# Optimization experiments

Measured on AMD Instinct MI355X. Metric: run time of the kernel, lower is better.

The kernel has to match this reference:

```python
import jax, jax.numpy as jnp
import numpy as np

B, S, V, E, H, T = 256, 160, 50000, 300, 256, 200

def setup_inputs() -> dict:
    key = jax.random.key(0)
    ks = jax.random.split(key, 12)
    return {
        'x1': jax.random.randint(ks[0], (B, S), 0, V),
        'x2': jax.random.randint(ks[1], (B, S), 0, V),
        'x1mask': jnp.ones((B, S), jnp.float32),
        'key_c': jax.random.normal(ks[2], (B, S, T), jnp.float32) * 0.1,
        'key_r': jax.random.normal(ks[3], (B, S, T), jnp.float32) * 0.1,
        'emb_table': jax.random.normal(ks[4], (V, E), jnp.float32) * 0.1,
        'W_ih': jax.random.normal(ks[5], (4 * H, E), jnp.float32) * 0.05,
        'W_hh': jax.random.normal(ks[6], (4 * H, H), jnp.float32) * 0.05,
        'W_kh': jax.random.normal(ks[7], (4 * H, T), jnp.float32) * 0.05,
        'b_g': jnp.zeros((4 * H,), jnp.float32),
        'W_attn': jax.random.normal(ks[8], (H, H), jnp.float32) * 0.05,
        'b_attn': jnp.zeros((H,), jnp.float32),
        'M': jax.random.normal(ks[9], (H, H), jnp.float32) * 0.05,
        'b': jnp.zeros((1,), jnp.float32),
    }

def _run_rnn(x_emb, k_emb, W_ih, W_hh, W_kh, b_g):
    # x_emb: [B,S,E], k_emb: [B,S,T] -> hidden states [B,S,H]
    Bn = x_emb.shape[0]
    h0 = jnp.zeros((Bn, H), x_emb.dtype)
    c0 = jnp.zeros((Bn, H), x_emb.dtype)
    def cell(carry, inp):
        h, c = carry
        x_t, k_t = inp
        g = x_t @ W_ih.T + h @ W_hh.T + k_t @ W_kh.T + b_g  # [B,4H]
        i, f, gg, o = jnp.split(g, 4, axis=-1)
        c = jax.nn.sigmoid(f) * c + jax.nn.sigmoid(i) * jnp.tanh(gg)
        h = jax.nn.sigmoid(o) * jnp.tanh(c)
        return (h, c), h
    xs = (jnp.swapaxes(x_emb, 0, 1), jnp.swapaxes(k_emb, 0, 1))  # time-major
    (_, _), hs = jax.lax.scan(cell, (h0, c0), xs)
    return jnp.swapaxes(hs, 0, 1)  # [B,S,H]

def reference(x1, x2, x1mask, key_c, key_r, emb_table, W_ih, W_hh, W_kh, b_g,
              W_attn, b_attn, M, b):
    x1_emb = emb_table[x1]  # [B,S,E] (dropout = identity at eval)
    x2_emb = emb_table[x2]
    sc = _run_rnn(x1_emb, key_c, W_ih, W_hh, W_kh, b_g)  # context states [B,S,H]
    rs = _run_rnn(x2_emb, key_r, W_ih, W_hh, W_kh, b_g)
    r = rs[:, -1]  # last response hidden [B,H]
    # masked dot-product attention over context states keyed by r
    attn = sc @ W_attn.T + b_attn  # [B,S,H]
    energies = jnp.einsum('bsh,bh->bs', attn, r) * x1mask
    alpha = jax.nn.softmax(energies, axis=-1)
    c_attn = jnp.einsum('bs,bsh->bh', alpha, sc)
    # bilinear score
    o = jnp.einsum('bh,hk,bk->b', c_attn, M, r) + b[0]
    return o
```

## Files before the change

kernel.cpp:

```cpp
#include <hip/hip_runtime.h>
#include <math.h>

#define B_   256
#define S_   160
#define E_   300
#define H_   256
#define T_   200
#define G4H  1024
#define CH   16
#define NCH  10

typedef float  f32x4  __attribute__((ext_vector_type(4)));
typedef __bf16 bf16x4 __attribute__((ext_vector_type(4)));
typedef __bf16 bf16x8 __attribute__((ext_vector_type(8)));

__device__ __forceinline__ float sigf(float x) {
    float e = expf(-fabsf(x));
    float p = 1.0f / (1.0f + e);
    return x >= 0.0f ? p : e * p;
}

__device__ __forceinline__ int norig(int np) {
    return ((np >> 4) & 3) * 256 + ((np >> 6) << 4) + (np & 15);
}

__device__ __forceinline__ float4 pick4(const float* __restrict__ e,
                                        const float* __restrict__ k, int kg) {
    if (kg < E_)      return *(const float4*)(e + kg);
    if (kg < E_ + T_) return *(const float4*)(k + (kg - E_));
    return make_float4(0.f, 0.f, 0.f, 0.f);
}

__device__ __forceinline__ void split4(float4 v, bf16x4& h, bf16x4& l) {
    h[0] = (__bf16)v.x; l[0] = (__bf16)(v.x - (float)h[0]);
    h[1] = (__bf16)v.y; l[1] = (__bf16)(v.y - (float)h[1]);
    h[2] = (__bf16)v.z; l[2] = (__bf16)(v.z - (float)h[2]);
    h[3] = (__bf16)v.w; l[3] = (__bf16)(v.w - (float)h[3]);
}

__global__ __launch_bounds__(128) void prep_split(
    const float* __restrict__ Whh, const float* __restrict__ Wih,
    const float* __restrict__ Wkh,
    __bf16* __restrict__ whh_hi, __bf16* __restrict__ whh_lo,
    __bf16* __restrict__ wik_hi, __bf16* __restrict__ wik_lo)
{
    const int n  = blockIdx.x;
    const int np = ((n & 255) >> 4) * 64 + (n >> 8) * 16 + (n & 15);
    const int t  = threadIdx.x;
    {
        const int k4 = t * 4;
        float4 v;
        if (k4 < E_)            v = *(const float4*)(Wih + (size_t)n * E_ + k4);
        else if (k4 < E_ + T_)  v = *(const float4*)(Wkh + (size_t)n * T_ + (k4 - E_));
        else                    v = make_float4(0.f, 0.f, 0.f, 0.f);
        bf16x4 h, l;
        split4(v, h, l);
        *(bf16x4*)(wik_hi + (size_t)np * 512 + k4) = h;
        *(bf16x4*)(wik_lo + (size_t)np * 512 + k4) = l;
    }
    if (t < 64) {
        const int k4 = t * 4;
        const float4 v = *(const float4*)(Whh + (size_t)n * 256 + k4);
        bf16x4 h, l;
        split4(v, h, l);
        *(bf16x4*)(whh_hi + (size_t)np * 256 + k4) = h;
        *(bf16x4*)(whh_lo + (size_t)np * 256 + k4) = l;
    }
}

__global__ __launch_bounds__(512, 2) void gemm_g2(
    const int* __restrict__ x1, const int* __restrict__ x2,
    const float* __restrict__ key_c, const float* __restrict__ key_r,
    const float* __restrict__ emb,
    const __bf16* __restrict__ wik_hi, const __bf16* __restrict__ wik_lo,
    const float* __restrict__ bg,
    float* __restrict__ G, int s0)
{
    __shared__ __align__(16) __bf16 Ah[128 * 32];
    __shared__ __align__(16) __bf16 Al[128 * 32];
    __shared__ __align__(16) __bf16 Bh[128 * 32];
    __shared__ __align__(16) __bf16 Bl[128 * 32];

    const int t   = threadIdx.x;
    const int rnn = blockIdx.z;
    const int m0  = blockIdx.x * 128;
    const int n0  = blockIdx.y * 128;
    const int* xx = rnn ? x2 : x1;
    const float* key = rnn ? key_r : key_c;

    const int r0 = t >> 2;
    const int cq = t & 3;
    const int csw = ((cq ^ ((r0 >> 1) & 3)) * 16);

    const float* aeb; const float* akb;
    const __bf16* wph; const __bf16* wpl;
    {
        const int am = m0 + r0;
        const int bs = (am >> 4) * S_ + s0 + (am & 15);
        aeb = emb + (size_t)xx[bs] * E_;
        akb = key + (size_t)bs * T_;
        wph = wik_hi + (size_t)(n0 + r0) * 512;
        wpl = wik_lo + (size_t)(n0 + r0) * 512;
    }

    const int w  = t >> 6;
    const int wm = w >> 2;
    const int wn = w & 3;
    const int l  = t & 63;
    const int cl = l & 15;
    const int ch = l >> 4;
    const int chs = ((ch ^ ((cl >> 1) & 3)) * 16);

    f32x4 acc[4][2];
    #pragma unroll
    for (int fm = 0; fm < 4; ++fm)
        #pragma unroll
        for (int fn = 0; fn < 2; ++fn) acc[fm][fn] = (f32x4){0.f, 0.f, 0.f, 0.f};

    for (int kt = 0; kt < 16; ++kt) {
        const int kg = kt * 32 + cq * 8;
        const float4 va0 = pick4(aeb, akb, kg);
        const float4 va1 = pick4(aeb, akb, kg + 4);
        const bf16x8 vbh = *(const bf16x8*)(wph + kg);
        const bf16x8 vbl = *(const bf16x8*)(wpl + kg);
        bf16x4 h0, l0, h1, l1;
        split4(va0, h0, l0);
        split4(va1, h1, l1);
        const bf16x8 sah = __builtin_shufflevector(h0, h1, 0, 1, 2, 3, 4, 5, 6, 7);
        const bf16x8 sal = __builtin_shufflevector(l0, l1, 0, 1, 2, 3, 4, 5, 6, 7);
        __syncthreads();
        {
            const int off = r0 * 64 + csw;
            *(bf16x8*)((char*)Ah + off) = sah;
            *(bf16x8*)((char*)Al + off) = sal;
            *(bf16x8*)((char*)Bh + off) = vbh;
            *(bf16x8*)((char*)Bl + off) = vbl;
        }
        __syncthreads();

        bf16x8 fBh[2], fBl[2];
        #pragma unroll
        for (int fn = 0; fn < 2; ++fn) {
            const int off = (wn * 32 + fn * 16 + cl) * 64 + chs;
            fBh[fn] = *(const bf16x8*)((const char*)Bh + off);
            fBl[fn] = *(const bf16x8*)((const char*)Bl + off);
        }
        #pragma unroll
        for (int fm = 0; fm < 4; ++fm) {
            const int off = (wm * 64 + fm * 16 + cl) * 64 + chs;
            const bf16x8 fAh = *(const bf16x8*)((const char*)Ah + off);
            const bf16x8 fAl = *(const bf16x8*)((const char*)Al + off);
            #pragma unroll
            for (int fn = 0; fn < 2; ++fn) {
                acc[fm][fn] = __builtin_amdgcn_mfma_f32_16x16x32_bf16(fAh, fBh[fn], acc[fm][fn], 0, 0, 0);
                acc[fm][fn] = __builtin_amdgcn_mfma_f32_16x16x32_bf16(fAh, fBl[fn], acc[fm][fn], 0, 0, 0);
                acc[fm][fn] = __builtin_amdgcn_mfma_f32_16x16x32_bf16(fAl, fBh[fn], acc[fm][fn], 0, 0, 0);
            }
        }
    }

    float bgl[2];
    #pragma unroll
    for (int fn = 0; fn < 2; ++fn)
        bgl[fn] = bg[norig(n0 + wn * 32 + fn * 16 + cl)];

    #pragma unroll
    for (int fm = 0; fm < 4; ++fm) {
        #pragma unroll
        for (int r = 0; r < 4; ++r) {
            const int m  = m0 + wm * 64 + fm * 16 + ch * 4 + r;
            const int b  = m >> 4;
            const int sl = m & 15;
            float* rowp = G + ((size_t)(rnn * CH + sl) * B_ + b) * G4H;
            #pragma unroll
            for (int fn = 0; fn < 2; ++fn)
                rowp[n0 + wn * 32 + fn * 16 + cl] = acc[fm][fn][r] + bgl[fn];
        }
    }
}

__global__ __launch_bounds__(256, 2) void lstm_ks(
    const float* __restrict__ G,
    const __bf16* __restrict__ Whi, const __bf16* __restrict__ Wlo,
    const __bf16* __restrict__ hhi_in, const __bf16* __restrict__ hlo_in,
    __bf16* __restrict__ hhi_out, __bf16* __restrict__ hlo_out,
    float* __restrict__ cst, float* __restrict__ sc,
    int sl, int s_glob, int first)
{
    __shared__ float ps[64 * 66];

    const int t  = threadIdx.x;
    const int w  = t >> 6;
    const int l  = t & 63;
    const int cl = l & 15;
    const int ch = l >> 4;
    const int mt = blockIdx.x;
    const int jt = blockIdx.y;
    const int rnn = mt >> 4;
    const int b0  = (mt & 15) * 16;
    const int m0  = mt * 16;

    const int me = t >> 4;
    const int jl = t & 15;
    const int j  = jt * 16 + jl;
    float Ge[4];
    const float* Gb = G + ((size_t)(rnn * CH + sl) * B_ + b0 + me) * G4H + jt * 64;
    #pragma unroll
    for (int g = 0; g < 4; ++g) Ge[g] = Gb[g * 16 + jl];
    const float c_in = first ? 0.f : cst[(size_t)(m0 + me) * 256 + j];

    const size_t ab = (size_t)(m0 + cl) * 256 + w * 64 + ch * 8;
    const bf16x8 fAh0 = *(const bf16x8*)(hhi_in + ab);
    const bf16x8 fAh1 = *(const bf16x8*)(hhi_in + ab + 32);
    const bf16x8 fAl0 = *(const bf16x8*)(hlo_in + ab);
    const bf16x8 fAl1 = *(const bf16x8*)(hlo_in + ab + 32);

    bf16x8 fBh[4][2], fBl[4][2];
    #pragma unroll
    for (int g = 0; g < 4; ++g) {
        const size_t bb = (size_t)(jt * 64 + g * 16 + cl) * 256 + w * 64 + ch * 8;
        fBh[g][0] = *(const bf16x8*)(Whi + bb);
        fBh[g][1] = *(const bf16x8*)(Whi + bb + 32);
        fBl[g][0] = *(const bf16x8*)(Wlo + bb);
        fBl[g][1] = *(const bf16x8*)(Wlo + bb + 32);
    }

    f32x4 acc[4];
    #pragma unroll
    for (int g = 0; g < 4; ++g) acc[g] = (f32x4){0.f, 0.f, 0.f, 0.f};
    #pragma unroll
    for (int g = 0; g < 4; ++g) {
        acc[g] = __builtin_amdgcn_mfma_f32_16x16x32_bf16(fAh0, fBh[g][0], acc[g], 0, 0, 0);
        acc[g] = __builtin_amdgcn_mfma_f32_16x16x32_bf16(fAh1, fBh[g][1], acc[g], 0, 0, 0);
        acc[g] = __builtin_amdgcn_mfma_f32_16x16x32_bf16(fAh0, fBl[g][0], acc[g], 0, 0, 0);
        acc[g] = __builtin_amdgcn_mfma_f32_16x16x32_bf16(fAh1, fBl[g][1], acc[g], 0, 0, 0);
        acc[g] = __builtin_amdgcn_mfma_f32_16x16x32_bf16(fAl0, fBh[g][0], acc[g], 0, 0, 0);
        acc[g] = __builtin_amdgcn_mfma_f32_16x16x32_bf16(fAl1, fBh[g][1], acc[g], 0, 0, 0);
    }

    #pragma unroll
    for (int g = 0; g < 4; ++g)
        #pragma unroll
        for (int r = 0; r < 4; ++r)
            ps[(w * 16 + ch * 4 + r) * 66 + g * 16 + cl] = acc[g][r];
    __syncthreads();

    float g4[4];
    #pragma unroll
    for (int g = 0; g < 4; ++g) {
        float s = Ge[g];
        #pragma unroll
        for (int w2 = 0; w2 < 4; ++w2)
            s += ps[(w2 * 16 + me) * 66 + g * 16 + jl];
        g4[g] = s;
    }
    const float c = sigf(g4[1]) * c_in + sigf(g4[0]) * tanhf(g4[2]);
    const float h = sigf(g4[3]) * tanhf(c);
    cst[(size_t)(m0 + me) * 256 + j] = c;
    const __bf16 hh = (__bf16)h;
    const size_t ho = (size_t)(m0 + me) * 256 + j;
    hhi_out[ho] = hh;
    hlo_out[ho] = (__bf16)(h - (float)hh);
    if (rnn == 0)
        sc[((size_t)(b0 + me) * S_ + s_glob) * H_ + j] = h;
}

__global__ __launch_bounds__(256) void final_kernel(
    const float* __restrict__ sc,
    const __bf16* __restrict__ rhi, const __bf16* __restrict__ rlo,
    const float* __restrict__ Wattn, const float* __restrict__ battn,
    const float* __restrict__ M, const float* __restrict__ bscal,
    const float* __restrict__ mask, float* __restrict__ out)
{
    __shared__ float rs[256], us[256], red[256], as_[256];
    const int b = blockIdx.x;
    const int t = threadIdx.x;

    const size_t ri = (size_t)(256 + b) * 256 + t;
    rs[t] = (float)rhi[ri] + (float)rlo[ri];
    __syncthreads();

    float acc = 0.0f;
    for (int h = 0; h < 256; ++h) acc += rs[h] * Wattn[h * 256 + t];
    us[t] = acc;

    red[t] = battn[t] * rs[t];
    __syncthreads();
    for (int off = 128; off; off >>= 1) {
        if (t < off) red[t] += red[t + off];
        __syncthreads();
    }
    float beta = red[0];
    __syncthreads();

    float vh = 0.0f;
    {
        const float* Mrow = M + t * 256;
        for (int k = 0; k < 256; ++k) vh += Mrow[k] * rs[k];
    }

    float e = -INFINITY;
    if (t < S_) {
        float d = 0.0f;
        const float* scrow = sc + ((size_t)b * S_ + t) * H_;
        for (int h = 0; h < 256; ++h) d += scrow[h] * us[h];
        e = (d + beta) * mask[b * S_ + t];
    }
    red[t] = e;
    __syncthreads();
    for (int off = 128; off; off >>= 1) {
        if (t < off) red[t] = fmaxf(red[t], red[t + off]);
        __syncthreads();
    }
    float mx = red[0];
    __syncthreads();

    float p = (t < S_) ? expf(e - mx) : 0.0f;
    as_[t] = p;
    red[t] = p;
    __syncthreads();
    for (int off = 128; off; off >>= 1) {
        if (t < off) red[t] += red[t + off];
        __syncthreads();
    }
    float inv = 1.0f / red[0];
    __syncthreads();

    float ca = 0.0f;
    for (int s = 0; s < S_; ++s) ca += as_[s] * sc[((size_t)b * S_ + s) * H_ + t];
    ca *= inv;

    red[t] = ca * vh;
    __syncthreads();
    for (int off = 128; off; off >>= 1) {
        if (t < off) red[t] += red[t + off];
        __syncthreads();
    }
    if (t == 0) out[b] = red[0] + bscal[0];
}

extern "C" void kernel_launch(void* const* d_in, const int* in_sizes, int n_in,
                              void* d_out, int out_size, void* d_ws, size_t ws_size,
                              hipStream_t stream)
{
    const int*   x1    = (const int*)d_in[0];
    const int*   x2    = (const int*)d_in[1];
    const float* mask  = (const float*)d_in[2];
    const float* key_c = (const float*)d_in[3];
    const float* key_r = (const float*)d_in[4];
    const float* emb   = (const float*)d_in[5];
    const float* Wih   = (const float*)d_in[6];
    const float* Whh   = (const float*)d_in[7];
    const float* Wkh   = (const float*)d_in[8];
    const float* bg    = (const float*)d_in[9];
    const float* Wattn = (const float*)d_in[10];
    const float* battn = (const float*)d_in[11];
    const float* M     = (const float*)d_in[12];
    const float* bb    = (const float*)d_in[13];
    float* out = (float*)d_out;
    char*  wsb = (char*)d_ws;

    float*  G     = (float*)(wsb + 0);
    float*  sc    = (float*)(wsb + 33554432);
    __bf16* hhi0  = (__bf16*)(wsb + 75497472);
    __bf16* hlo0  = (__bf16*)(wsb + 75759616);
    __bf16* hhi1  = (__bf16*)(wsb + 76021760);
    __bf16* hlo1  = (__bf16*)(wsb + 76283904);
    float*  cst   = (float*)(wsb + 76546048);
    __bf16* WhhHi = (__bf16*)(wsb + 77070336);
    __bf16* WhhLo = (__bf16*)(wsb + 77594624);
    __bf16* WikHi = (__bf16*)(wsb + 78118912);
    __bf16* WikLo = (__bf16*)(wsb + 79167488);
    if (ws_size < 80216064) return;

    hipMemsetAsync(hhi0, 0, 524288, stream);
    prep_split<<<dim3(1024), 128, 0, stream>>>(Whh, Wih, Wkh,
                                               WhhHi, WhhLo, WikHi, WikLo);

    for (int ci = 0; ci < NCH; ++ci) {
        gemm_g2<<<dim3(32, 8, 2), 512, 0, stream>>>(x1, x2, key_c, key_r, emb,
                                                    WikHi, WikLo, bg, G, ci * CH);
        for (int slq = 0; slq < CH; ++slq) {
            const int s   = ci * CH + slq;
            const int par = s & 1;
            lstm_ks<<<dim3(32, 16), 256, 0, stream>>>(G, WhhHi, WhhLo,
                                                      par ? hhi1 : hhi0,
                                                      par ? hlo1 : hlo0,
                                                      par ? hhi0 : hhi1,
                                                      par ? hlo0 : hlo1,
                                                      cst, sc, slq, s, s == 0);
        }
    }

    final_kernel<<<dim3(256), 256, 0, stream>>>(sc, hhi0, hlo0, Wattn, battn,
                                                M, bb, mask, out);
}
```

Baseline: 1.473 ms.

## Fuse input-projection GEMM slices into recurrent step kernels via ring buffer

Replaces the chunked schedule, which ran one big input-projection GEMM per 16 steps followed by 16 recurrent-step launches, with a boot GEMM for the first 16 timesteps. After that, each step launch also computes the input projection for timestep t+16 in extra blocks, writing into a 17-slot ring buffer. The goal is to hide the GEMM work inside the latency-bound recurrent steps, which use only 512 blocks, and to remove the separate GEMM launches. The GEMM tile shrinks to 64x64 with 256 threads. The risk is that the extra GEMM blocks compete with the critical-path LSTM blocks for compute units and slow each step.

```diff
diff --git a/kernel.cpp b/kernel.cpp
--- a/kernel.cpp
+++ b/kernel.cpp
@@ -9,6 +9,9 @@
 #define G4H  1024
 #define CH   16
 #define NCH  10
+#define NSTEP 160
+#define NSLOT 17
+#define SLICE_F 524288
 
 typedef float  f32x4  __attribute__((ext_vector_type(4)));
 typedef __bf16 bf16x4 __attribute__((ext_vector_type(4)));
@@ -68,52 +71,46 @@
     }
 }
 
-__global__ __launch_bounds__(512, 2) void gemm_g2(
+__device__ __forceinline__ void dev_gemm_slice(
+    char* smem, int mx, int ny, int rnn, int s_tgt,
     const int* __restrict__ x1, const int* __restrict__ x2,
     const float* __restrict__ key_c, const float* __restrict__ key_r,
     const float* __restrict__ emb,
     const __bf16* __restrict__ wik_hi, const __bf16* __restrict__ wik_lo,
-    const float* __restrict__ bg,
-    float* __restrict__ G, int s0)
-{
-    __shared__ __align__(16) __bf16 Ah[128 * 32];
-    __shared__ __align__(16) __bf16 Al[128 * 32];
-    __shared__ __align__(16) __bf16 Bh[128 * 32];
-    __shared__ __align__(16) __bf16 Bl[128 * 32];
-
-    const int t   = threadIdx.x;
-    const int rnn = blockIdx.z;
-    const int m0  = blockIdx.x * 128;
-    const int n0  = blockIdx.y * 128;
+    const float* __restrict__ bg, float* __restrict__ Gw)
+{
+    __bf16* Ah = (__bf16*)smem;
+    __bf16* Al = Ah + 64 * 32;
+    __bf16* Bh = Al + 64 * 32;
+    __bf16* Bl = Bh + 64 * 32;
+
+    const int t  = threadIdx.x;
+    const int m0 = mx * 64;
+    const int n0 = ny * 64;
     const int* xx = rnn ? x2 : x1;
     const float* key = rnn ? key_r : key_c;
 
-    const int r0 = t >> 2;
-    const int cq = t & 3;
+    const int r0  = t >> 2;
+    const int cq  = t & 3;
     const int csw = ((cq ^ ((r0 >> 1) & 3)) * 16);
 
-    const float* aeb; const float* akb;
-    const __bf16* wph; const __bf16* wpl;
-    {
-        const int am = m0 + r0;
-        const int bs = (am >> 4) * S_ + s0 + (am & 15);
-        aeb = emb + (size_t)xx[bs] * E_;
-        akb = key + (size_t)bs * T_;
-        wph = wik_hi + (size_t)(n0 + r0) * 512;
-        wpl = wik_lo + (size_t)(n0 + r0) * 512;
-    }
+    const int bs = (m0 + r0) * S_ + s_tgt;
+    const float* aeb = emb + (size_t)xx[bs] * E_;
+    const float* akb = key + (size_t)bs * T_;
+    const __bf16* wph = wik_hi + (size_t)(n0 + r0) * 512;
+    const __bf16* wpl = wik_lo + (size_t)(n0 + r0) * 512;
 
     const int w  = t >> 6;
-    const int wm = w >> 2;
-    const int wn = w & 3;
+    const int wm = w >> 1;
+    const int wn = w & 1;
     const int l  = t & 63;
     const int cl = l & 15;
     const int ch = l >> 4;
     const int chs = ((ch ^ ((cl >> 1) & 3)) * 16);
 
-    f32x4 acc[4][2];
-    #pragma unroll
-    for (int fm = 0; fm < 4; ++fm)
+    f32x4 acc[2][2];
+    #pragma unroll
+    for (int fm = 0; fm < 2; ++fm)
         #pragma unroll
         for (int fn = 0; fn < 2; ++fn) acc[fm][fn] = (f32x4){0.f, 0.f, 0.f, 0.f};
 
@@ -146,8 +143,8 @@
             fBl[fn] = *(const bf16x8*)((const char*)Bl + off);
         }
         #pragma unroll
-        for (int fm = 0; fm < 4; ++fm) {
-            const int off = (wm * 64 + fm * 16 + cl) * 64 + chs;
+        for (int fm = 0; fm < 2; ++fm) {
+            const int off = (wm * 32 + fm * 16 + cl) * 64 + chs;
             const bf16x8 fAh = *(const bf16x8*)((const char*)Ah + off);
             const bf16x8 fAl = *(const bf16x8*)((const char*)Al + off);
             #pragma unroll
@@ -165,13 +162,11 @@
         bgl[fn] = bg[norig(n0 + wn * 32 + fn * 16 + cl)];
 
     #pragma unroll
-    for (int fm = 0; fm < 4; ++fm) {
+    for (int fm = 0; fm < 2; ++fm) {
         #pragma unroll
         for (int r = 0; r < 4; ++r) {
-            const int m  = m0 + wm * 64 + fm * 16 + ch * 4 + r;
-            const int b  = m >> 4;
-            const int sl = m & 15;
-            float* rowp = G + ((size_t)(rnn * CH + sl) * B_ + b) * G4H;
+            const int b = m0 + wm * 32 + fm * 16 + ch * 4 + r;
+            float* rowp = Gw + ((size_t)rnn * 256 + b) * G4H;
             #pragma unroll
             for (int fn = 0; fn < 2; ++fn)
                 rowp[n0 + wn * 32 + fn * 16 + cl] = acc[fm][fn][r] + bgl[fn];
@@ -179,23 +174,22 @@
     }
 }
 
-__global__ __launch_bounds__(256, 2) void lstm_ks(
-    const float* __restrict__ G,
+__device__ __forceinline__ void dev_lstm_step(
+    char* smem, int mt, int jt,
+    const float* __restrict__ Gread,
     const __bf16* __restrict__ Whi, const __bf16* __restrict__ Wlo,
     const __bf16* __restrict__ hhi_in, const __bf16* __restrict__ hlo_in,
     __bf16* __restrict__ hhi_out, __bf16* __restrict__ hlo_out,
     float* __restrict__ cst, float* __restrict__ sc,
-    int sl, int s_glob, int first)
-{
-    __shared__ float ps[64 * 66];
+    int s_glob, int first)
+{
+    float* ps = (float*)smem;
 
     const int t  = threadIdx.x;
     const int w  = t >> 6;
     const int l  = t & 63;
     const int cl = l & 15;
     const int ch = l >> 4;
-    const int mt = blockIdx.x;
-    const int jt = blockIdx.y;
     const int rnn = mt >> 4;
     const int b0  = (mt & 15) * 16;
     const int m0  = mt * 16;
@@ -204,7 +198,7 @@
     const int jl = t & 15;
     const int j  = jt * 16 + jl;
     float Ge[4];
-    const float* Gb = G + ((size_t)(rnn * CH + sl) * B_ + b0 + me) * G4H + jt * 64;
+    const float* Gb = Gread + (size_t)(m0 + me) * G4H + jt * 64;
     #pragma unroll
     for (int g = 0; g < 4; ++g) Ge[g] = Gb[g * 16 + jl];
     const float c_in = first ? 0.f : cst[(size_t)(m0 + me) * 256 + j];
@@ -263,6 +257,48 @@
     hlo_out[ho] = (__bf16)(h - (float)hh);
     if (rnn == 0)
         sc[((size_t)(b0 + me) * S_ + s_glob) * H_ + j] = h;
+}
+
+__global__ __launch_bounds__(256, 3) void gemm_boot(
+    const int* __restrict__ x1, const int* __restrict__ x2,
+    const float* __restrict__ key_c, const float* __restrict__ key_r,
+    const float* __restrict__ emb,
+    const __bf16* __restrict__ wik_hi, const __bf16* __restrict__ wik_lo,
+    const float* __restrict__ bg, float* __restrict__ Gbase)
+{
+    __shared__ __align__(16) char smem[16896];
+    const int q  = blockIdx.x;
+    const int sl = q >> 7;
+    const int gb = q & 127;
+    dev_gemm_slice(smem, gb & 3, (gb >> 2) & 15, gb >> 6, sl,
+                   x1, x2, key_c, key_r, emb, wik_hi, wik_lo, bg,
+                   Gbase + (size_t)sl * SLICE_F);
+}
+
+__global__ __launch_bounds__(256, 3) void fused_step(
+    const float* __restrict__ Gread, float* __restrict__ Gwrite,
+    const __bf16* __restrict__ Whi, const __bf16* __restrict__ Wlo,
+    const __bf16* __restrict__ hhi_in, const __bf16* __restrict__ hlo_in,
+    __bf16* __restrict__ hhi_out, __bf16* __restrict__ hlo_out,
+    float* __restrict__ cst, float* __restrict__ sc,
+    const int* __restrict__ x1, const int* __restrict__ x2,
+    const float* __restrict__ key_c, const float* __restrict__ key_r,
+    const float* __restrict__ emb,
+    const __bf16* __restrict__ wik_hi, const __bf16* __restrict__ wik_lo,
+    const float* __restrict__ bg,
+    int s_glob, int first, int do_gemm)
+{
+    __shared__ __align__(16) char smem[16896];
+    const int bid = blockIdx.x;
+    if (bid < 512) {
+        dev_lstm_step(smem, bid & 31, bid >> 5, Gread, Whi, Wlo,
+                      hhi_in, hlo_in, hhi_out, hlo_out, cst, sc,
+                      s_glob, first);
+    } else if (do_gemm) {
+        const int gb = bid - 512;
+        dev_gemm_slice(smem, gb & 3, (gb >> 2) & 15, gb >> 6, s_glob + 16,
+                       x1, x2, key_c, key_r, emb, wik_hi, wik_lo, bg, Gwrite);
+    }
 }
 
 __global__ __launch_bounds__(256) void final_kernel(
@@ -361,35 +397,35 @@
     char*  wsb = (char*)d_ws;
 
     float*  G     = (float*)(wsb + 0);
-    float*  sc    = (float*)(wsb + 33554432);
-    __bf16* hhi0  = (__bf16*)(wsb + 75497472);
-    __bf16* hlo0  = (__bf16*)(wsb + 75759616);
-    __bf16* hhi1  = (__bf16*)(wsb + 76021760);
-    __bf16* hlo1  = (__bf16*)(wsb + 76283904);
-    float*  cst   = (float*)(wsb + 76546048);
-    __bf16* WhhHi = (__bf16*)(wsb + 77070336);
-    __bf16* WhhLo = (__bf16*)(wsb + 77594624);
-    __bf16* WikHi = (__bf16*)(wsb + 78118912);
-    __bf16* WikLo = (__bf16*)(wsb + 79167488);
-    if (ws_size < 80216064) return;
+    float*  sc    = (float*)(wsb + 35651584);
+    __bf16* hhi0  = (__bf16*)(wsb + 77594624);
+    __bf16* hlo0  = (__bf16*)(wsb + 77856768);
+    __bf16* hhi1  = (__bf16*)(wsb + 78118912);
+    __bf16* hlo1  = (__bf16*)(wsb + 78381056);
+    float*  cst   = (float*)(wsb + 78643200);
+    __bf16* WhhHi = (__bf16*)(wsb + 79167488);
+    __bf16* WhhLo = (__bf16*)(wsb + 79691776);
+    __bf16* WikHi = (__bf16*)(wsb + 80216064);
+    __bf16* WikLo = (__bf16*)(wsb + 81264640);
+    if (ws_size < 82313216) return;
 
     hipMemsetAsync(hhi0, 0, 524288, stream);
     prep_split<<<dim3(1024), 128, 0, stream>>>(Whh, Wih, Wkh,
                                                WhhHi, WhhLo, WikHi, WikLo);
-
-    for (int ci = 0; ci < NCH; ++ci) {
-        gemm_g2<<<dim3(32, 8, 2), 512, 0, stream>>>(x1, x2, key_c, key_r, emb,
-                                                    WikHi, WikLo, bg, G, ci * CH);
-        for (int slq = 0; slq < CH; ++slq) {
-            const int s   = ci * CH + slq;
-            const int par = s & 1;
-            lstm_ks<<<dim3(32, 16), 256, 0, stream>>>(G, WhhHi, WhhLo,
-                                                      par ? hhi1 : hhi0,
-                                                      par ? hlo1 : hlo0,
-                                                      par ? hhi0 : hhi1,
-                                                      par ? hlo0 : hlo1,
-                                                      cst, sc, slq, s, s == 0);
-        }
+    gemm_boot<<<dim3(2048), 256, 0, stream>>>(x1, x2, key_c, key_r, emb,
+                                              WikHi, WikLo, bg, G);
+
+    for (int t = 0; t < NSTEP; ++t) {
+        const int par = t & 1;
+        fused_step<<<dim3(640), 256, 0, stream>>>(
+            G + (size_t)(t % NSLOT) * SLICE_F,
+            G + (size_t)((t + 16) % NSLOT) * SLICE_F,
+            WhhHi, WhhLo,
+            par ? hhi1 : hhi0, par ? hlo1 : hlo0,
+            par ? hhi0 : hhi1, par ? hlo0 : hlo1,
+            cst, sc,
+            x1, x2, key_c, key_r, emb, WikHi, WikLo, bg,
+            t, t == 0, (t + 16) < NSTEP);
     }
 
     final_kernel<<<dim3(256), 256, 0, stream>>>(sc, hhi0, hlo0, Wattn, battn,
```

After: 3.124 ms. 2.12x slower.
